# Kernel optimization log

Measured on AMD Instinct MI355X. Metric: run time of the kernel, lower is better.

The kernel has to match this reference:

```python
import jax, jax.numpy as jnp
import numpy as np

NHEAD, D_K, D_V, D_MODEL = 16, 64, 64, 1024
B, LQ, LK = 2, 2048, 2048
LN_EPS = 1e-6


def setup_inputs() -> dict:
    key = jax.random.key(0)
    ks = jax.random.split(key, 12)
    s = 0.02
    return {
        "q": jax.random.normal(ks[0], (B, LQ, D_MODEL), jnp.float32),
        "k": jax.random.normal(ks[1], (B, LK, D_MODEL), jnp.float32),
        "v": jax.random.normal(ks[2], (B, LK, D_MODEL), jnp.float32),
        "mask": jax.random.randint(ks[3], (B, LQ, LK), 0, 2, jnp.int32),
        "mean": jax.random.uniform(ks[4], (B, LK), jnp.float32, 0.5, 1.5),
        "std": jax.random.uniform(ks[5], (B, LK), jnp.float32, -0.5, 0.5),
        "w_qs": jax.random.normal(ks[6], (D_MODEL, NHEAD * D_K), jnp.float32) * s,
        "w_ks": jax.random.normal(ks[7], (D_MODEL, NHEAD * D_K), jnp.float32) * s,
        "w_vs": jax.random.normal(ks[8], (D_MODEL, NHEAD * D_V), jnp.float32) * s,
        "w_fc": jax.random.normal(ks[9], (NHEAD * D_V, D_MODEL), jnp.float32) * s,
        "ln_gamma": jnp.ones((D_MODEL,), jnp.float32),
        "ln_beta": jnp.zeros((D_MODEL,), jnp.float32),
    }


def _layer_norm(x, gamma, beta):
    mu = jnp.mean(x, axis=-1, keepdims=True)
    var = jnp.mean(jnp.square(x - mu), axis=-1, keepdims=True)
    return (x - mu) * jax.lax.rsqrt(var + LN_EPS) * gamma + beta


def reference(q, k, v, mask, mean, std, w_qs, w_ks, w_vs, w_fc, ln_gamma, ln_beta):
    residual = q
    # projections -> [B, H, L, d]
    qh = (q @ w_qs).reshape(B, LQ, NHEAD, D_K).transpose(0, 2, 1, 3)
    kh = (k @ w_ks).reshape(B, LK, NHEAD, D_K).transpose(0, 2, 1, 3)
    vh = (v @ w_vs).reshape(B, LK, NHEAD, D_V).transpose(0, 2, 1, 3)
    # scores with affine modification: (QK^T * mean + std) / sqrt(d_k)
    attn = jnp.einsum("bhqd,bhkd->bhqk", qh, kh)
    attn = (attn * mean[:, None, None, :] + std[:, None, None, :]) / jnp.sqrt(jnp.float32(D_K))
    attn = jnp.where(mask[:, None, :, :] == 0, jnp.float32(-1e9), attn)
    attn = jax.nn.softmax(attn, axis=-1)
    out = jnp.einsum("bhqk,bhkd->bhqd", attn, vh)  # [B,H,Lq,Dv]
    out = out.transpose(0, 2, 1, 3).reshape(B, LQ, NHEAD * D_V)
    out = out @ w_fc + residual
    return _layer_norm(out, ln_gamma, ln_beta)
```

## Files before the change

### kernel.cpp

```cpp
#include <hip/hip_runtime.h>
#include <math.h>

#define NHEAD 16
#define DK 64
#define DMODEL 1024
#define BB 2
#define LQ 2048
#define LK 2048
#define MROWS (BB * LQ)
#define PLANE ((size_t)MROWS * DMODEL)
#define WPLANE ((size_t)DMODEL * DMODEL)

typedef __attribute__((ext_vector_type(8))) short short8v;
typedef __attribute__((ext_vector_type(4))) float f32x4;
typedef __attribute__((ext_vector_type(16))) float f32x16;
typedef __attribute__((ext_vector_type(4))) uint uint4v;

__device__ __forceinline__ ushort f2bf(float x) {
  uint u = __builtin_bit_cast(uint, x);
  u += 0x7FFFu + ((u >> 16) & 1u);
  return (ushort)(u >> 16);
}
__device__ __forceinline__ float bf2f(ushort h) {
  return __builtin_bit_cast(float, ((uint)h) << 16);
}

__global__ __launch_bounds__(256) void conv_x3(
    const float* __restrict__ q, const float* __restrict__ k,
    const float* __restrict__ v, ushort* __restrict__ hiB,
    ushort* __restrict__ loB, int n4) {
  const int z = blockIdx.z;
  const float* x = z == 0 ? q : z == 1 ? k : v;
  ushort* hi = hiB + (size_t)z * PLANE;
  ushort* lo = loB + (size_t)z * PLANE;
  for (int i = blockIdx.x * blockDim.x + threadIdx.x; i < n4;
       i += gridDim.x * blockDim.x) {
    float4 vv = ((const float4*)x)[i];
    ushort4 h, l;
    h.x = f2bf(vv.x); l.x = f2bf(vv.x - bf2f(h.x));
    h.y = f2bf(vv.y); l.y = f2bf(vv.y - bf2f(h.y));
    h.z = f2bf(vv.z); l.z = f2bf(vv.z - bf2f(h.z));
    h.w = f2bf(vv.w); l.w = f2bf(vv.w - bf2f(h.w));
    ((ushort4*)hi)[i] = h;
    ((ushort4*)lo)[i] = l;
  }
}

__global__ __launch_bounds__(256) void conv_wT(
    const float* __restrict__ w0, const float* __restrict__ w1,
    const float* __restrict__ w2, const float* __restrict__ w3,
    ushort* __restrict__ hiB, ushort* __restrict__ loB) {
  const float* W = blockIdx.z == 0 ? w0
                   : blockIdx.z == 1 ? w1
                   : blockIdx.z == 2 ? w2 : w3;
  ushort* hi = hiB + (size_t)blockIdx.z * WPLANE;
  ushort* lo = loB + (size_t)blockIdx.z * WPLANE;
  __shared__ ushort Th[64][66], Tl[64][66];
  const int t = threadIdx.x;
  const int n0 = blockIdx.x * 64, k0 = blockIdx.y * 64;
  const int r = t >> 4, c4 = (t & 15) << 2;
#pragma unroll
  for (int p = 0; p < 4; ++p) {
    const int kr = r + p * 16;
    float4 v = *(const float4*)&W[(size_t)(k0 + kr) * DMODEL + n0 + c4];
    ushort h;
    h = f2bf(v.x); Th[c4 + 0][kr] = h; Tl[c4 + 0][kr] = f2bf(v.x - bf2f(h));
    h = f2bf(v.y); Th[c4 + 1][kr] = h; Tl[c4 + 1][kr] = f2bf(v.y - bf2f(h));
    h = f2bf(v.z); Th[c4 + 2][kr] = h; Tl[c4 + 2][kr] = f2bf(v.z - bf2f(h));
    h = f2bf(v.w); Th[c4 + 3][kr] = h; Tl[c4 + 3][kr] = f2bf(v.w - bf2f(h));
  }
  __syncthreads();
  const int n = t >> 2, g = t & 3;
  uint uh[8], ul[8];
#pragma unroll
  for (int j = 0; j < 8; ++j) {
    uh[j] = *(const uint*)&Th[n][g * 16 + 2 * j];
    ul[j] = *(const uint*)&Tl[n][g * 16 + 2 * j];
  }
  const size_t ob = (size_t)(n0 + n) * DMODEL + k0 + g * 16;
  *(uint4*)&hi[ob] = make_uint4(uh[0], uh[1], uh[2], uh[3]);
  *(uint4*)&hi[ob + 8] = make_uint4(uh[4], uh[5], uh[6], uh[7]);
  *(uint4*)&lo[ob] = make_uint4(ul[0], ul[1], ul[2], ul[3]);
  *(uint4*)&lo[ob + 8] = make_uint4(ul[4], ul[5], ul[6], ul[7]);
}

template <int MODE>
__global__ __launch_bounds__(256, 2) void gemm_mfma(
    const ushort* __restrict__ Ah, const ushort* __restrict__ Al,
    const ushort* __restrict__ Bh, const ushort* __restrict__ Bl,
    ushort* __restrict__ Oh, ushort* __restrict__ Ol,
    float* __restrict__ outF, const float* __restrict__ res) {
  __shared__ __align__(16) ushort As_hi[128 * 32], As_lo[128 * 32];
  __shared__ __align__(16) ushort Bs_hi[128 * 32], Bs_lo[128 * 32];

  const int t = threadIdx.x;
  const int ln = t & 63, wv = t >> 6;
  const int wm = wv >> 1, wn = wv & 1;
  const int n0 = blockIdx.x * 128, m0 = blockIdx.y * 128;
  const int zz = blockIdx.z;

  if (MODE == 3) {
    Ah += (size_t)zz * PLANE;  Al += (size_t)zz * PLANE;
    Bh += (size_t)zz * WPLANE; Bl += (size_t)zz * WPLANE;
    Oh += (size_t)zz * PLANE;  Ol += (size_t)zz * PLANE;
  }

  const int am = t & 127, akg = t >> 7;
  const int bn = am, bkg = akg;

  const ushort* Aph = Ah + (size_t)(m0 + am) * 1024 + akg * 16;
  const ushort* Apl = Al + (size_t)(m0 + am) * 1024 + akg * 16;
  const ushort* Bph = Bh + (size_t)(n0 + bn) * 1024 + bkg * 16;
  const ushort* Bpl = Bl + (size_t)(n0 + bn) * 1024 + bkg * 16;

  short8v ah0 = *(const short8v*)(Aph), ah1 = *(const short8v*)(Aph + 8);
  short8v al0 = *(const short8v*)(Apl), al1 = *(const short8v*)(Apl + 8);
  short8v bh0 = *(const short8v*)(Bph), bh1 = *(const short8v*)(Bph + 8);
  short8v bl0 = *(const short8v*)(Bpl), bl1 = *(const short8v*)(Bpl + 8);

  f32x4 acc[4][4];
#pragma unroll
  for (int i = 0; i < 4; ++i)
#pragma unroll
    for (int j = 0; j < 4; ++j)
#pragma unroll
      for (int r = 0; r < 4; ++r) acc[i][j][r] = 0.f;

  const int swa = (am >> 1) & 3;
  const int s0 = (akg * 2) ^ swa, s1 = (akg * 2 + 1) ^ swa;

  for (int k0 = 0; k0 < 1024; k0 += 32) {
    __syncthreads();
    *(short8v*)&As_hi[am * 32 + s0 * 8] = ah0;
    *(short8v*)&As_hi[am * 32 + s1 * 8] = ah1;
    *(short8v*)&As_lo[am * 32 + s0 * 8] = al0;
    *(short8v*)&As_lo[am * 32 + s1 * 8] = al1;
    *(short8v*)&Bs_hi[bn * 32 + s0 * 8] = bh0;
    *(short8v*)&Bs_hi[bn * 32 + s1 * 8] = bh1;
    *(short8v*)&Bs_lo[bn * 32 + s0 * 8] = bl0;
    *(short8v*)&Bs_lo[bn * 32 + s1 * 8] = bl1;
    __syncthreads();

    if (k0 + 32 < 1024) {
      ah0 = *(const short8v*)(Aph + k0 + 32);
      ah1 = *(const short8v*)(Aph + k0 + 40);
      al0 = *(const short8v*)(Apl + k0 + 32);
      al1 = *(const short8v*)(Apl + k0 + 40);
      bh0 = *(const short8v*)(Bph + k0 + 32);
      bh1 = *(const short8v*)(Bph + k0 + 40);
      bl0 = *(const short8v*)(Bpl + k0 + 32);
      bl1 = *(const short8v*)(Bpl + k0 + 40);
    }

    short8v fah[4], fal[4], fbh[4], fbl[4];
#pragma unroll
    for (int mf = 0; mf < 4; ++mf) {
      const int mr = wm * 64 + mf * 16 + (ln & 15);
      const int sl = (ln >> 4) ^ ((mr >> 1) & 3);
      fah[mf] = *(const short8v*)&As_hi[mr * 32 + sl * 8];
      fal[mf] = *(const short8v*)&As_lo[mr * 32 + sl * 8];
    }
#pragma unroll
    for (int nf = 0; nf < 4; ++nf) {
      const int nr = wn * 64 + nf * 16 + (ln & 15);
      const int sl = (ln >> 4) ^ ((nr >> 1) & 3);
      fbh[nf] = *(const short8v*)&Bs_hi[nr * 32 + sl * 8];
      fbl[nf] = *(const short8v*)&Bs_lo[nr * 32 + sl * 8];
    }
#pragma unroll
    for (int mi = 0; mi < 4; ++mi)
#pragma unroll
      for (int ni = 0; ni < 4; ++ni) {
        acc[mi][ni] = __builtin_amdgcn_mfma_f32_16x16x32_bf16(
            fah[mi], fbh[ni], acc[mi][ni], 0, 0, 0);
        acc[mi][ni] = __builtin_amdgcn_mfma_f32_16x16x32_bf16(
            fal[mi], fbh[ni], acc[mi][ni], 0, 0, 0);
        acc[mi][ni] = __builtin_amdgcn_mfma_f32_16x16x32_bf16(
            fah[mi], fbl[ni], acc[mi][ni], 0, 0, 0);
      }
  }

#pragma unroll
  for (int mi = 0; mi < 4; ++mi)
#pragma unroll
    for (int ni = 0; ni < 4; ++ni) {
      const int ng = n0 + wn * 64 + ni * 16 + (ln & 15);
#pragma unroll
      for (int r = 0; r < 4; ++r) {
        const int mg = m0 + wm * 64 + mi * 16 + (ln >> 4) * 4 + r;
        const float val = acc[mi][ni][r];
        if (MODE == 1) {
          outF[(size_t)mg * 1024 + ng] = val + res[(size_t)mg * 1024 + ng];
        } else {
          const int h = ng >> 6, d = ng & 63;
          const int bb = mg >> 11, l = mg & (LQ - 1);
          size_t idx;
          if (zz == 2) idx = ((size_t)(bb * NHEAD + h) * 64 + d) * LK + l;
          else         idx = ((size_t)(bb * NHEAD + h) * LQ + l) * 64 + d;
          const ushort hb = f2bf(val);
          Oh[idx] = hb;
          Ol[idx] = f2bf(val - bf2f(hb));
        }
      }
    }
}

__global__ __launch_bounds__(256, 2) void attn_mfma(
    const ushort* __restrict__ Qhh, const ushort* __restrict__ Qhl,
    const ushort* __restrict__ Khh, const ushort* __restrict__ Khl,
    const ushort* __restrict__ VTh, const ushort* __restrict__ VTl,
    const int* __restrict__ mask, const float* __restrict__ mean,
    const float* __restrict__ stdv, ushort* __restrict__ AOh,
    ushort* __restrict__ AOl) {
  __shared__ __align__(16) ushort Ks_hi[32 * 64], Ks_lo[32 * 64];
  __shared__ __align__(16) ushort VT_hi[64 * 40], VT_lo[64 * 40];
  __shared__ float sc_lds[4][32];

  const int t = threadIdx.x;
  const int w = t >> 6, ln = t & 63;
  const int lq = ln & 31;
  const int hi5 = ln >> 5;

  const int q0 = blockIdx.x * 128 + w * 32;
  const int h = blockIdx.y, b = blockIdx.z;

  const size_t hb_ = (size_t)(b * NHEAD + h);
  const ushort* Qh_ = Qhh + hb_ * LQ * 64;
  const ushort* Ql_ = Qhl + hb_ * LQ * 64;
  const ushort* Kh_ = Khh + hb_ * LK * 64;
  const ushort* Kl_ = Khl + hb_ * LK * 64;
  const ushort* Vh_ = VTh + hb_ * 64 * LK;
  const ushort* Vl_ = VTl + hb_ * 64 * LK;

  short8v qf_h[4], qf_l[4];
#pragma unroll
  for (int ds = 0; ds < 4; ++ds) {
    const size_t off = (size_t)(q0 + lq) * 64 + ds * 16 + hi5 * 8;
    qf_h[ds] = *(const short8v*)&Qh_[off];
    qf_l[ds] = *(const short8v*)&Ql_[off];
  }

  const int skr = t >> 3, sds = t & 7;
  const int vd = t >> 2, vg = t & 3;
  const int kslot = sds ^ (skr & 7);

  short8v kp_h = *(const short8v*)&Kh_[(size_t)skr * 64 + sds * 8];
  short8v kp_l = *(const short8v*)&Kl_[(size_t)skr * 64 + sds * 8];
  short8v vp_h = *(const short8v*)&Vh_[(size_t)vd * LK + vg * 8];
  short8v vp_l = *(const short8v*)&Vl_[(size_t)vd * LK + vg * 8];

  f32x16 Oa[2];
#pragma unroll
  for (int dt = 0; dt < 2; ++dt)
#pragma unroll
    for (int r = 0; r < 16; ++r) Oa[dt][r] = 0.f;
  float mrun = -INFINITY, lrun = 0.f;

  for (int k0 = 0; k0 < LK; k0 += 32) {
    __syncthreads();
    *(short8v*)&Ks_hi[skr * 64 + kslot * 8] = kp_h;
    *(short8v*)&Ks_lo[skr * 64 + kslot * 8] = kp_l;
    *(short8v*)&VT_hi[vd * 40 + vg * 8] = vp_h;
    *(short8v*)&VT_lo[vd * 40 + vg * 8] = vp_l;
    __syncthreads();

    float4 mn[4], sd[4];
    int4 mk[4];
#pragma unroll
    for (int g = 0; g < 4; ++g) {
      const int kb = k0 + 8 * g + 4 * hi5;
      mn[g] = *(const float4*)&mean[(size_t)b * LK + kb];
      sd[g] = *(const float4*)&stdv[(size_t)b * LK + kb];
      mk[g] = *(const int4*)&mask[((size_t)b * LQ + q0 + lq) * LK + kb];
    }

    if (k0 + 32 < LK) {
      kp_h = *(const short8v*)&Kh_[(size_t)(k0 + 32 + skr) * 64 + sds * 8];
      kp_l = *(const short8v*)&Kl_[(size_t)(k0 + 32 + skr) * 64 + sds * 8];
      vp_h = *(const short8v*)&Vh_[(size_t)vd * LK + k0 + 32 + vg * 8];
      vp_l = *(const short8v*)&Vl_[(size_t)vd * LK + k0 + 32 + vg * 8];
    }

    f32x16 S;
#pragma unroll
    for (int r = 0; r < 16; ++r) S[r] = 0.f;
#pragma unroll
    for (int ds = 0; ds < 4; ++ds) {
      const int dsl = (ds * 2 + hi5) ^ (lq & 7);
      short8v kf_h = *(const short8v*)&Ks_hi[lq * 64 + dsl * 8];
      short8v kf_l = *(const short8v*)&Ks_lo[lq * 64 + dsl * 8];
      S = __builtin_amdgcn_mfma_f32_32x32x16_bf16(kf_h, qf_h[ds], S, 0, 0, 0);
      S = __builtin_amdgcn_mfma_f32_32x32x16_bf16(kf_l, qf_h[ds], S, 0, 0, 0);
      S = __builtin_amdgcn_mfma_f32_32x32x16_bf16(kf_h, qf_l[ds], S, 0, 0, 0);
    }

    float p[16];
    float tmax = -INFINITY;
#pragma unroll
    for (int r = 0; r < 16; ++r) {
      const int g = r >> 2, j = r & 3;
      float v = fmaf(S[r], ((const float*)&mn[g])[j] * 0.125f,
                     ((const float*)&sd[g])[j] * 0.125f);
      v = (((const int*)&mk[g])[j] == 0) ? -1e9f : v;
      p[r] = v;
      tmax = fmaxf(tmax, v);
    }
    tmax = fmaxf(tmax, __shfl_xor(tmax, 32, 64));
    const bool need = __any(tmax > mrun);
    const float mnew = need ? fmaxf(mrun, tmax) : mrun;
    float psum = 0.f;
#pragma unroll
    for (int r = 0; r < 16; ++r) {
      p[r] = __expf(p[r] - mnew);
      psum += p[r];
    }
    psum += __shfl_xor(psum, 32, 64);
    if (need) {
      const float scl = __expf(mrun - mnew);
      lrun = lrun * scl + psum;
      mrun = mnew;
      sc_lds[w][lq] = scl;
      float4 s4[4];
#pragma unroll
      for (int g = 0; g < 4; ++g)
        s4[g] = *(const float4*)&sc_lds[w][8 * g + 4 * hi5];
#pragma unroll
      for (int dt = 0; dt < 2; ++dt)
#pragma unroll
        for (int r = 0; r < 16; ++r)
          Oa[dt][r] *= ((const float*)&s4[r >> 2])[r & 3];
    } else {
      lrun += psum;
    }

    uint ch[8], cl[8];
#pragma unroll
    for (int j = 0; j < 8; ++j) {
      const float a = p[2 * j], c = p[2 * j + 1];
      const ushort h0 = __builtin_bit_cast(ushort, (__bf16)a);
      const ushort h1 = __builtin_bit_cast(ushort, (__bf16)c);
      ch[j] = (uint)h0 | ((uint)h1 << 16);
      const float l0 = a - bf2f(h0);
      const float l1 = c - bf2f(h1);
      const ushort g0 = __builtin_bit_cast(ushort, (__bf16)l0);
      const ushort g1 = __builtin_bit_cast(ushort, (__bf16)l1);
      cl[j] = (uint)g0 | ((uint)g1 << 16);
    }
    asm("v_permlane32_swap_b32 %0, %1" : "+v"(ch[0]), "+v"(ch[2]));
    asm("v_permlane32_swap_b32 %0, %1" : "+v"(ch[1]), "+v"(ch[3]));
    asm("v_permlane32_swap_b32 %0, %1" : "+v"(ch[4]), "+v"(ch[6]));
    asm("v_permlane32_swap_b32 %0, %1" : "+v"(ch[5]), "+v"(ch[7]));
    asm("v_permlane32_swap_b32 %0, %1" : "+v"(cl[0]), "+v"(cl[2]));
    asm("v_permlane32_swap_b32 %0, %1" : "+v"(cl[1]), "+v"(cl[3]));
    asm("v_permlane32_swap_b32 %0, %1" : "+v"(cl[4]), "+v"(cl[6]));
    asm("v_permlane32_swap_b32 %0, %1" : "+v"(cl[5]), "+v"(cl[7]));
    short8v paH[2], paL[2];
    {
      uint4v u;
      u = (uint4v){ch[0], ch[1], ch[2], ch[3]};
      paH[0] = __builtin_bit_cast(short8v, u);
      u = (uint4v){ch[4], ch[5], ch[6], ch[7]};
      paH[1] = __builtin_bit_cast(short8v, u);
      u = (uint4v){cl[0], cl[1], cl[2], cl[3]};
      paL[0] = __builtin_bit_cast(short8v, u);
      u = (uint4v){cl[4], cl[5], cl[6], cl[7]};
      paL[1] = __builtin_bit_cast(short8v, u);
    }

#pragma unroll
    for (int dt = 0; dt < 2; ++dt)
#pragma unroll
      for (int ki = 0; ki < 2; ++ki) {
        short8v vbh =
            *(const short8v*)&VT_hi[(dt * 32 + lq) * 40 + ki * 16 + hi5 * 8];
        short8v vbl =
            *(const short8v*)&VT_lo[(dt * 32 + lq) * 40 + ki * 16 + hi5 * 8];
        Oa[dt] = __builtin_amdgcn_mfma_f32_32x32x16_bf16(paH[ki], vbh, Oa[dt], 0, 0, 0);
        Oa[dt] = __builtin_amdgcn_mfma_f32_32x32x16_bf16(paL[ki], vbh, Oa[dt], 0, 0, 0);
        Oa[dt] = __builtin_amdgcn_mfma_f32_32x32x16_bf16(paH[ki], vbl, Oa[dt], 0, 0, 0);
      }
  }

  sc_lds[w][lq] = 1.0f / lrun;
  float4 iv[4];
#pragma unroll
  for (int g = 0; g < 4; ++g)
    iv[g] = *(const float4*)&sc_lds[w][8 * g + 4 * hi5];
#pragma unroll
  for (int dt = 0; dt < 2; ++dt)
#pragma unroll
    for (int r = 0; r < 16; ++r) {
      const int ql = (r & 3) + 8 * (r >> 2) + 4 * hi5;
      const float v = Oa[dt][r] * ((const float*)&iv[r >> 2])[r & 3];
      const size_t idx =
          (size_t)(b * LQ + q0 + ql) * DMODEL + h * 64 + dt * 32 + lq;
      const ushort hbv = f2bf(v);
      AOh[idx] = hbv;
      AOl[idx] = f2bf(v - bf2f(hbv));
    }
}

__global__ __launch_bounds__(256) void ln_kernel(float* __restrict__ io,
                                                 const float* __restrict__ gamma,
                                                 const float* __restrict__ beta) {
  const int row = blockIdx.x;
  const int t = threadIdx.x;
  float* base = io + (size_t)row * DMODEL;
  float4 x = *(const float4*)&base[t << 2];
  float s = x.x + x.y + x.z + x.w;
#pragma unroll
  for (int xm = 1; xm < 64; xm <<= 1) s += __shfl_xor(s, xm, 64);
  __shared__ float part[4];
  __shared__ float smu, svar;
  if ((t & 63) == 0) part[t >> 6] = s;
  __syncthreads();
  if (t == 0) smu = (part[0] + part[1] + part[2] + part[3]) * (1.0f / DMODEL);
  __syncthreads();
  const float mu = smu;
  const float d0 = x.x - mu, d1 = x.y - mu, d2 = x.z - mu, d3 = x.w - mu;
  float s2 = d0 * d0 + d1 * d1 + d2 * d2 + d3 * d3;
#pragma unroll
  for (int xm = 1; xm < 64; xm <<= 1) s2 += __shfl_xor(s2, xm, 64);
  if ((t & 63) == 0) part[t >> 6] = s2;
  __syncthreads();
  if (t == 0) svar = (part[0] + part[1] + part[2] + part[3]) * (1.0f / DMODEL);
  __syncthreads();
  const float inv = rsqrtf(svar + 1e-6f);
  float4 g = *(const float4*)&gamma[t << 2];
  float4 be = *(const float4*)&beta[t << 2];
  float4 o;
  o.x = d0 * inv * g.x + be.x;
  o.y = d1 * inv * g.y + be.y;
  o.z = d2 * inv * g.z + be.z;
  o.w = d3 * inv * g.w + be.w;
  *(float4*)&base[t << 2] = o;
}

extern "C" void kernel_launch(void* const* d_in, const int* in_sizes, int n_in,
                              void* d_out, int out_size, void* d_ws,
                              size_t ws_size, hipStream_t stream) {
  const float* q = (const float*)d_in[0];
  const float* k = (const float*)d_in[1];
  const float* v = (const float*)d_in[2];
  const int* mask = (const int*)d_in[3];
  const float* mean = (const float*)d_in[4];
  const float* stdv = (const float*)d_in[5];
  const float* w_qs = (const float*)d_in[6];
  const float* w_ks = (const float*)d_in[7];
  const float* w_vs = (const float*)d_in[8];
  const float* w_fc = (const float*)d_in[9];
  const float* gamma = (const float*)d_in[10];
  const float* beta = (const float*)d_in[11];
  float* out = (float*)d_out;

  ushort* xinH = (ushort*)d_ws;
  ushort* xinL = xinH + 3 * PLANE;
  ushort* prH  = xinL + 3 * PLANE;
  ushort* prL  = prH + 3 * PLANE;
  ushort* wT_h = prL + 3 * PLANE;
  ushort* wT_l = wT_h + 4 * WPLANE;
  ushort* aoH = xinH;
  ushort* aoL = xinL;

  dim3 blk(256);
  const int n4 = MROWS * DMODEL / 4;

  conv_wT<<<dim3(16, 16, 4), blk, 0, stream>>>(w_qs, w_ks, w_vs, w_fc, wT_h, wT_l);
  conv_x3<<<dim3(512, 1, 3), blk, 0, stream>>>(q, k, v, xinH, xinL, n4);

  gemm_mfma<3><<<dim3(8, 32, 3), blk, 0, stream>>>(
      xinH, xinL, wT_h, wT_l, prH, prL, nullptr, nullptr);

  attn_mfma<<<dim3(16, 16, 2), blk, 0, stream>>>(
      prH, prL, prH + PLANE, prL + PLANE, prH + 2 * PLANE, prL + 2 * PLANE,
      mask, mean, stdv, aoH, aoL);

  gemm_mfma<1><<<dim3(8, 32), blk, 0, stream>>>(
      aoH, aoL, wT_h + 3 * WPLANE, wT_l + 3 * WPLANE, nullptr, nullptr, out, q);
  ln_kernel<<<MROWS, blk, 0, stream>>>(out, gamma, beta);
}
```

Baseline: 519.5 us.

## Split attention over key halves, bit-pack mask, double-buffer K/V tiles

```diff
diff --git a/kernel.cpp b/kernel.cpp
--- a/kernel.cpp
+++ b/kernel.cpp
@@ -23,6 +23,19 @@
 }
 __device__ __forceinline__ float bf2f(ushort h) {
   return __builtin_bit_cast(float, ((uint)h) << 16);
+}
+
+__global__ __launch_bounds__(256) void pack_mask(const int* __restrict__ mask,
+                                                 uint* __restrict__ bits) {
+  const int nPairs = BB * LQ * (LK / 32) / 2;
+  const int wid = threadIdx.x >> 6, ln = threadIdx.x & 63;
+  const int nw = gridDim.x * 4;
+  for (int p = blockIdx.x * 4 + wid; p < nPairs; p += nw) {
+    const int m = mask[(size_t)p * 64 + ln];
+    unsigned long long bal = __ballot(m != 0);
+    if (ln == 0) bits[p * 2] = (uint)bal;
+    if (ln == 32) bits[p * 2 + 1] = (uint)(bal >> 32);
+  }
 }
 
 __global__ __launch_bounds__(256) void conv_x3(
@@ -106,12 +119,11 @@
   }
 
   const int am = t & 127, akg = t >> 7;
-  const int bn = am, bkg = akg;
 
   const ushort* Aph = Ah + (size_t)(m0 + am) * 1024 + akg * 16;
   const ushort* Apl = Al + (size_t)(m0 + am) * 1024 + akg * 16;
-  const ushort* Bph = Bh + (size_t)(n0 + bn) * 1024 + bkg * 16;
-  const ushort* Bpl = Bl + (size_t)(n0 + bn) * 1024 + bkg * 16;
+  const ushort* Bph = Bh + (size_t)(n0 + am) * 1024 + akg * 16;
+  const ushort* Bpl = Bl + (size_t)(n0 + am) * 1024 + akg * 16;
 
   short8v ah0 = *(const short8v*)(Aph), ah1 = *(const short8v*)(Aph + 8);
   short8v al0 = *(const short8v*)(Apl), al1 = *(const short8v*)(Apl + 8);
@@ -135,10 +147,10 @@
     *(short8v*)&As_hi[am * 32 + s1 * 8] = ah1;
     *(short8v*)&As_lo[am * 32 + s0 * 8] = al0;
     *(short8v*)&As_lo[am * 32 + s1 * 8] = al1;
-    *(short8v*)&Bs_hi[bn * 32 + s0 * 8] = bh0;
-    *(short8v*)&Bs_hi[bn * 32 + s1 * 8] = bh1;
-    *(short8v*)&Bs_lo[bn * 32 + s0 * 8] = bl0;
-    *(short8v*)&Bs_lo[bn * 32 + s1 * 8] = bl1;
+    *(short8v*)&Bs_hi[am * 32 + s0 * 8] = bh0;
+    *(short8v*)&Bs_hi[am * 32 + s1 * 8] = bh1;
+    *(short8v*)&Bs_lo[am * 32 + s0 * 8] = bl0;
+    *(short8v*)&Bs_lo[am * 32 + s1 * 8] = bl1;
     __syncthreads();
 
     if (k0 + 32 < 1024) {
@@ -205,15 +217,15 @@
     }
 }
 
-__global__ __launch_bounds__(256, 2) void attn_mfma(
+__global__ __launch_bounds__(256, 4) void attn_mfma(
     const ushort* __restrict__ Qhh, const ushort* __restrict__ Qhl,
     const ushort* __restrict__ Khh, const ushort* __restrict__ Khl,
     const ushort* __restrict__ VTh, const ushort* __restrict__ VTl,
-    const int* __restrict__ mask, const float* __restrict__ mean,
-    const float* __restrict__ stdv, ushort* __restrict__ AOh,
-    ushort* __restrict__ AOl) {
-  __shared__ __align__(16) ushort Ks_hi[32 * 64], Ks_lo[32 * 64];
-  __shared__ __align__(16) ushort VT_hi[64 * 40], VT_lo[64 * 40];
+    const uint* __restrict__ mbits, const float* __restrict__ mean,
+    const float* __restrict__ stdv, float* __restrict__ Opart,
+    float* __restrict__ MLpart) {
+  __shared__ __align__(16) ushort Ks_hi[2][32 * 64], Ks_lo[2][32 * 64];
+  __shared__ __align__(16) ushort VT_hi[2][64 * 40], VT_lo[2][64 * 40];
   __shared__ float sc_lds[4][32];
 
   const int t = threadIdx.x;
@@ -222,15 +234,21 @@
   const int hi5 = ln >> 5;
 
   const int q0 = blockIdx.x * 128 + w * 32;
-  const int h = blockIdx.y, b = blockIdx.z;
+  const int h = blockIdx.y;
+  const int bz = blockIdx.z, b = bz >> 1, kh = bz & 1;
+  const int kbase = kh * (LK / 2);
+  const int NIT = (LK / 2) / 32;
+
+  Opart += (size_t)kh * PLANE;
+  MLpart += (size_t)kh * ((size_t)BB * NHEAD * LQ * 2);
 
   const size_t hb_ = (size_t)(b * NHEAD + h);
   const ushort* Qh_ = Qhh + hb_ * LQ * 64;
   const ushort* Ql_ = Qhl + hb_ * LQ * 64;
-  const ushort* Kh_ = Khh + hb_ * LK * 64;
-  const ushort* Kl_ = Khl + hb_ * LK * 64;
-  const ushort* Vh_ = VTh + hb_ * 64 * LK;
-  const ushort* Vl_ = VTl + hb_ * 64 * LK;
+  const ushort* Kh_ = Khh + hb_ * LK * 64 + (size_t)kbase * 64;
+  const ushort* Kl_ = Khl + hb_ * LK * 64 + (size_t)kbase * 64;
+  const ushort* Vh_ = VTh + hb_ * 64 * LK + kbase;
+  const ushort* Vl_ = VTl + hb_ * 64 * LK + kbase;
 
   short8v qf_h[4], qf_l[4];
 #pragma unroll
@@ -248,6 +266,11 @@
   short8v kp_l = *(const short8v*)&Kl_[(size_t)skr * 64 + sds * 8];
   short8v vp_h = *(const short8v*)&Vh_[(size_t)vd * LK + vg * 8];
   short8v vp_l = *(const short8v*)&Vl_[(size_t)vd * LK + vg * 8];
+  *(short8v*)&Ks_hi[0][skr * 64 + kslot * 8] = kp_h;
+  *(short8v*)&Ks_lo[0][skr * 64 + kslot * 8] = kp_l;
+  *(short8v*)&VT_hi[0][vd * 40 + vg * 8] = vp_h;
+  *(short8v*)&VT_lo[0][vd * 40 + vg * 8] = vp_l;
+  __syncthreads();
 
   f32x16 Oa[2];
 #pragma unroll
@@ -256,29 +279,27 @@
     for (int r = 0; r < 16; ++r) Oa[dt][r] = 0.f;
   float mrun = -INFINITY, lrun = 0.f;
 
-  for (int k0 = 0; k0 < LK; k0 += 32) {
-    __syncthreads();
-    *(short8v*)&Ks_hi[skr * 64 + kslot * 8] = kp_h;
-    *(short8v*)&Ks_lo[skr * 64 + kslot * 8] = kp_l;
-    *(short8v*)&VT_hi[vd * 40 + vg * 8] = vp_h;
-    *(short8v*)&VT_lo[vd * 40 + vg * 8] = vp_l;
-    __syncthreads();
-
+  const size_t mrow = ((size_t)(b * LQ + q0 + lq)) * 64 + kh * 32;
+
+  for (int it = 0; it < NIT; ++it) {
+    const int k0 = it * 32;
+    const int cur = it & 1;
+
+    const uint mw = mbits[mrow + it];
     float4 mn[4], sd[4];
-    int4 mk[4];
 #pragma unroll
     for (int g = 0; g < 4; ++g) {
-      const int kb = k0 + 8 * g + 4 * hi5;
+      const int kb = kbase + k0 + 8 * g + 4 * hi5;
       mn[g] = *(const float4*)&mean[(size_t)b * LK + kb];
       sd[g] = *(const float4*)&stdv[(size_t)b * LK + kb];
-      mk[g] = *(const int4*)&mask[((size_t)b * LQ + q0 + lq) * LK + kb];
-    }
-
-    if (k0 + 32 < LK) {
-      kp_h = *(const short8v*)&Kh_[(size_t)(k0 + 32 + skr) * 64 + sds * 8];
-      kp_l = *(const short8v*)&Kl_[(size_t)(k0 + 32 + skr) * 64 + sds * 8];
-      vp_h = *(const short8v*)&Vh_[(size_t)vd * LK + k0 + 32 + vg * 8];
-      vp_l = *(const short8v*)&Vl_[(size_t)vd * LK + k0 + 32 + vg * 8];
+    }
+
+    if (it + 1 < NIT) {
+      const int nk = k0 + 32;
+      kp_h = *(const short8v*)&Kh_[(size_t)(nk + skr) * 64 + sds * 8];
+      kp_l = *(const short8v*)&Kl_[(size_t)(nk + skr) * 64 + sds * 8];
+      vp_h = *(const short8v*)&Vh_[(size_t)vd * LK + nk + vg * 8];
+      vp_l = *(const short8v*)&Vl_[(size_t)vd * LK + nk + vg * 8];
     }
 
     f32x16 S;
@@ -287,8 +308,8 @@
 #pragma unroll
     for (int ds = 0; ds < 4; ++ds) {
       const int dsl = (ds * 2 + hi5) ^ (lq & 7);
-      short8v kf_h = *(const short8v*)&Ks_hi[lq * 64 + dsl * 8];
-      short8v kf_l = *(const short8v*)&Ks_lo[lq * 64 + dsl * 8];
+      short8v kf_h = *(const short8v*)&Ks_hi[cur][lq * 64 + dsl * 8];
+      short8v kf_l = *(const short8v*)&Ks_lo[cur][lq * 64 + dsl * 8];
       S = __builtin_amdgcn_mfma_f32_32x32x16_bf16(kf_h, qf_h[ds], S, 0, 0, 0);
       S = __builtin_amdgcn_mfma_f32_32x32x16_bf16(kf_l, qf_h[ds], S, 0, 0, 0);
       S = __builtin_amdgcn_mfma_f32_32x32x16_bf16(kf_h, qf_l[ds], S, 0, 0, 0);
@@ -299,9 +320,10 @@
 #pragma unroll
     for (int r = 0; r < 16; ++r) {
       const int g = r >> 2, j = r & 3;
+      const int kit = (r & 3) + 8 * (r >> 2) + 4 * hi5;
       float v = fmaf(S[r], ((const float*)&mn[g])[j] * 0.125f,
                      ((const float*)&sd[g])[j] * 0.125f);
-      v = (((const int*)&mk[g])[j] == 0) ? -1e9f : v;
+      v = ((mw >> kit) & 1u) ? v : -1e9f;
       p[r] = v;
       tmax = fmaxf(tmax, v);
     }
@@ -372,32 +394,64 @@
 #pragma unroll
       for (int ki = 0; ki < 2; ++ki) {
         short8v vbh =
-            *(const short8v*)&VT_hi[(dt * 32 + lq) * 40 + ki * 16 + hi5 * 8];
+            *(const short8v*)&VT_hi[cur][(dt * 32 + lq) * 40 + ki * 16 + hi5 * 8];
         short8v vbl =
-            *(const short8v*)&VT_lo[(dt * 32 + lq) * 40 + ki * 16 + hi5 * 8];
+            *(const short8v*)&VT_lo[cur][(dt * 32 + lq) * 40 + ki * 16 + hi5 * 8];
         Oa[dt] = __builtin_amdgcn_mfma_f32_32x32x16_bf16(paH[ki], vbh, Oa[dt], 0, 0, 0);
         Oa[dt] = __builtin_amdgcn_mfma_f32_32x32x16_bf16(paL[ki], vbh, Oa[dt], 0, 0, 0);
         Oa[dt] = __builtin_amdgcn_mfma_f32_32x32x16_bf16(paH[ki], vbl, Oa[dt], 0, 0, 0);
       }
-  }
-
-  sc_lds[w][lq] = 1.0f / lrun;
-  float4 iv[4];
-#pragma unroll
-  for (int g = 0; g < 4; ++g)
-    iv[g] = *(const float4*)&sc_lds[w][8 * g + 4 * hi5];
+
+    if (it + 1 < NIT) {
+      const int nxt = cur ^ 1;
+      *(short8v*)&Ks_hi[nxt][skr * 64 + kslot * 8] = kp_h;
+      *(short8v*)&Ks_lo[nxt][skr * 64 + kslot * 8] = kp_l;
+      *(short8v*)&VT_hi[nxt][vd * 40 + vg * 8] = vp_h;
+      *(short8v*)&VT_lo[nxt][vd * 40 + vg * 8] = vp_l;
+    }
+    __syncthreads();
+  }
+
+  if (hi5 == 0) {
+    const size_t mli = (hb_ * LQ + q0 + lq) * 2;
+    MLpart[mli] = mrun;
+    MLpart[mli + 1] = lrun;
+  }
 #pragma unroll
   for (int dt = 0; dt < 2; ++dt)
 #pragma unroll
     for (int r = 0; r < 16; ++r) {
       const int ql = (r & 3) + 8 * (r >> 2) + 4 * hi5;
-      const float v = Oa[dt][r] * ((const float*)&iv[r >> 2])[r & 3];
-      const size_t idx =
-          (size_t)(b * LQ + q0 + ql) * DMODEL + h * 64 + dt * 32 + lq;
-      const ushort hbv = f2bf(v);
-      AOh[idx] = hbv;
-      AOl[idx] = f2bf(v - bf2f(hbv));
-    }
+      Opart[(size_t)(b * LQ + q0 + ql) * DMODEL + h * 64 + dt * 32 + lq] =
+          Oa[dt][r];
+    }
+}
+
+__global__ __launch_bounds__(256) void merge_attn(
+    const float* __restrict__ O0, const float* __restrict__ O1,
+    const float* __restrict__ ML0, const float* __restrict__ ML1,
+    ushort* __restrict__ aoH, ushort* __restrict__ aoL) {
+  const int row = blockIdx.x, t = threadIdx.x;
+  const int d4 = t << 2, h = d4 >> 6;
+  const int b = row >> 11, q = row & (LQ - 1);
+  const size_t mli = ((size_t)(b * NHEAD + h) * LQ + q) * 2;
+  const float m0 = ML0[mli], l0 = ML0[mli + 1];
+  const float m1 = ML1[mli], l1 = ML1[mli + 1];
+  const float M = fmaxf(m0, m1);
+  const float a0 = __expf(m0 - M), a1 = __expf(m1 - M);
+  const float inv = 1.0f / (l0 * a0 + l1 * a1);
+  const size_t base = (size_t)row * DMODEL + d4;
+  float4 o0 = *(const float4*)&O0[base];
+  float4 o1 = *(const float4*)&O1[base];
+  float vx[4] = {(o0.x * a0 + o1.x * a1) * inv, (o0.y * a0 + o1.y * a1) * inv,
+                 (o0.z * a0 + o1.z * a1) * inv, (o0.w * a0 + o1.w * a1) * inv};
+  ushort4 hh, ll;
+  hh.x = f2bf(vx[0]); ll.x = f2bf(vx[0] - bf2f(hh.x));
+  hh.y = f2bf(vx[1]); ll.y = f2bf(vx[1] - bf2f(hh.y));
+  hh.z = f2bf(vx[2]); ll.z = f2bf(vx[2] - bf2f(hh.z));
+  hh.w = f2bf(vx[3]); ll.w = f2bf(vx[3] - bf2f(hh.w));
+  *(ushort4*)&aoH[base] = hh;
+  *(ushort4*)&aoL[base] = ll;
 }
 
 __global__ __launch_bounds__(256) void ln_kernel(float* __restrict__ io,
@@ -453,27 +507,35 @@
   const float* beta = (const float*)d_in[11];
   float* out = (float*)d_out;
 
-  ushort* xinH = (ushort*)d_ws;
-  ushort* xinL = xinH + 3 * PLANE;
-  ushort* prH  = xinL + 3 * PLANE;
-  ushort* prL  = prH + 3 * PLANE;
+  ushort* prH = (ushort*)d_ws;
+  ushort* prL = prH + 3 * PLANE;
   ushort* wT_h = prL + 3 * PLANE;
   ushort* wT_l = wT_h + 4 * WPLANE;
-  ushort* aoH = xinH;
-  ushort* aoL = xinL;
+  ushort* xinH = wT_l + 4 * WPLANE;
+  ushort* xinL = xinH + 3 * PLANE;
+  float* O0 = (float*)xinH;
+  float* O1 = O0 + PLANE;
+  ushort* aoH = (ushort*)(O1 + PLANE);
+  ushort* aoL = aoH + PLANE;
+  uint* mbits = (uint*)(xinL + 3 * PLANE);
+  float* ML0 = (float*)(mbits + (size_t)BB * LQ * 64);
+  float* ML1 = ML0 + (size_t)BB * NHEAD * LQ * 2;
 
   dim3 blk(256);
   const int n4 = MROWS * DMODEL / 4;
 
+  pack_mask<<<2048, blk, 0, stream>>>(mask, mbits);
   conv_wT<<<dim3(16, 16, 4), blk, 0, stream>>>(w_qs, w_ks, w_vs, w_fc, wT_h, wT_l);
   conv_x3<<<dim3(512, 1, 3), blk, 0, stream>>>(q, k, v, xinH, xinL, n4);
 
   gemm_mfma<3><<<dim3(8, 32, 3), blk, 0, stream>>>(
       xinH, xinL, wT_h, wT_l, prH, prL, nullptr, nullptr);
 
-  attn_mfma<<<dim3(16, 16, 2), blk, 0, stream>>>(
+  attn_mfma<<<dim3(16, 16, 2 * BB), blk, 0, stream>>>(
       prH, prL, prH + PLANE, prL + PLANE, prH + 2 * PLANE, prL + 2 * PLANE,
-      mask, mean, stdv, aoH, aoL);
+      mbits, mean, stdv, O0, ML0);
+
+  merge_attn<<<MROWS, blk, 0, stream>>>(O0, O1, ML0, ML1, aoH, aoL);
 
   gemm_mfma<1><<<dim3(8, 32), blk, 0, stream>>>(
       aoH, aoL, wT_h + 3 * WPLANE, wT_l + 3 * WPLANE, nullptr, nullptr, out, q);
```

New measurement: 695.0 us. 1.34x slower.
